# Optimization experiments

Hardware: AMD Instinct MI355X
Metric: run time of the kernel (lower is better)

The kernel has to match this reference:

```python
import jax, jax.numpy as jnp
import numpy as np

B, N, CS, CZ, H, CH, G, P = 2, 384, 384, 128, 8, 16, 2, 8
CZ4 = CZ // 4
INF = 1e5
UMAX = 3.0     # self.u_max
LMAX = 2.0     # self.log_scale_max
SQRT_CH = CH ** 0.5


def quat_to_rot(q):
    q = q / jnp.linalg.norm(q, axis=-1, keepdims=True)
    w, x, y, z = q[..., 0], q[..., 1], q[..., 2], q[..., 3]
    R = jnp.stack([
        1 - 2 * (y * y + z * z), 2 * (x * y - w * z), 2 * (x * z + w * y),
        2 * (x * y + w * z), 1 - 2 * (x * x + z * z), 2 * (y * z - w * x),
        2 * (x * z - w * y), 2 * (y * z + w * x), 1 - 2 * (x * x + y * y)], axis=-1)
    return R.reshape(q.shape[:-1] + (3, 3))


def robust_nll(delta, sigma):
    # inline robust 3x3 Cholesky solve: dist_sq = d^T S^-1 d, log_det = ln|S|
    eps = 1e-8
    s00 = sigma[..., 0, 0]; s01 = sigma[..., 0, 1]; s02 = sigma[..., 0, 2]
    s11 = sigma[..., 1, 1]; s12 = sigma[..., 1, 2]; s22 = sigma[..., 2, 2]
    d0 = delta[..., 0]; d1 = delta[..., 1]; d2 = delta[..., 2]
    l00_sq = jnp.maximum(s00, eps); inv_l00 = jax.lax.rsqrt(l00_sq)
    l10 = s01 * inv_l00; l20 = s02 * inv_l00
    l11_sq = jnp.maximum(s11 - l10 * l10, eps); inv_l11 = jax.lax.rsqrt(l11_sq)
    l21 = (s12 - l20 * l10) * inv_l11
    l22_sq = jnp.maximum(s22 - l20 * l20 - l21 * l21, eps); inv_l22 = jax.lax.rsqrt(l22_sq)
    log_det = jnp.log(l00_sq) + jnp.log(l11_sq) + jnp.log(l22_sq)
    y0 = d0 * inv_l00
    y1 = (d1 - l10 * y0) * inv_l11
    y2 = (d2 - l20 * y0 - l21 * y1) * inv_l22
    return y0 * y0 + y1 * y1 + y2 * y2, log_det


def iga_forward(s, z, mask, rot, trans, local_mean, scaling_log,
                Wq, Wk, Wv, Wb, bb, Wdz, bdz, Wqg, bqg, Wkg, bkg,
                Wvp, bvp, geo_scale, geo_bias, Wout, bout):
    # scalar q/k/v: [B,H,N,CH]
    q = (s @ Wq).reshape(B, N, H, CH).transpose(0, 2, 1, 3)
    k = (s @ Wk).reshape(B, N, H, CH).transpose(0, 2, 1, 3)
    v = (s @ Wv).reshape(B, N, H, CH).transpose(0, 2, 1, 3)
    logits = jnp.einsum('bhid,bhjd->bhij', q, k) / SQRT_CH
    # pair bias: [B,H,N,N]
    logits = logits + (z @ Wb + bb).transpose(0, 3, 1, 2)

    def parse(feat):  # -> u [B,N,H,G,3], s_log_delta [B,N,H,G,3]
        raw = feat.reshape(B, N, H, G, 6)
        return jnp.tanh(raw[..., :3]) * UMAX, jnp.tanh(raw[..., 3:]) * LMAX

    def to_global(u, sld):
        anchor = local_mean[:, :, None, None, :]
        base = scaling_log[:, :, None, None, :]
        sig_loc = jnp.maximum(jnp.exp(base + sld), 1e-6)
        pos = anchor + u * sig_loc
        mu = jnp.einsum('bnij,bnhgj->bnhgi', rot, pos) + trans[:, :, None, None, :]
        var = jnp.exp(2.0 * (base + sld))
        Sig = jnp.einsum('bnij,bnhgj,bnkj->bnhgik', rot, var, rot)  # R diag(var) R^T
        return mu.transpose(0, 2, 1, 3, 4), Sig.transpose(0, 2, 1, 3, 4, 5)

    qu, qs = parse(s @ Wqg + bqg)
    ku, ks = parse(s @ Wkg + bkg)
    q_mu, q_sig = to_global(qu, qs)   # [B,H,N,G,3], [B,H,N,G,3,3]
    k_mu, k_sig = to_global(ku, ks)
    delta = q_mu[:, :, :, None] - k_mu[:, :, None, :]      # [B,H,N,N,G,3]
    ssum = q_sig[:, :, :, None] + k_sig[:, :, None, :]     # [B,H,N,N,G,3,3]
    dist_sq, log_det = robust_nll(delta, ssum)
    geo = (-0.5 * dist_sq - 0.5 * log_det).sum(-1)          # [B,H,N,N]

    mask2d = mask[:, None, :, None] * mask[:, None, None, :]  # [B,1,N,N]
    a = jax.nn.softplus(geo_scale)[None, :, None, None]
    G_geo = a * (geo * mask2d) + geo_bias[None, :, None, None]
    logits = logits + G_geo + (1.0 - mask2d) * (-INF)
    w = jax.nn.softmax(logits, axis=-1)                      # [B,H,N,N]

    # scalar output
    o = jnp.einsum('bhij,bhjd->bihd', w, v).reshape(B, N, H * CH)
    # point output (IPA-style): to global, attend, back to local frame
    vpts = (s @ Wvp + bvp).reshape(B, N, H, P, 3)
    vpg = jnp.einsum('bnij,bnhpj->bnhpi', rot, vpts) + trans[:, :, None, None, :]
    vpg = vpg.transpose(0, 2, 1, 3, 4)                       # [B,H,N,P,3]
    opt = jnp.einsum('bhij,bhjpc->bhipc', w, vpg)            # [B,H,N,P,3]
    opt_local = jnp.einsum('bnji,bhnpj->bnhpi', rot, opt - trans[:, None, :, None, :])
    onorm = jnp.sqrt((opt_local ** 2).sum(-1) + 1e-8)        # [B,N,H,P]
    # pair output
    pz = z @ Wdz + bdz                                       # [B,N,N,CZ4]
    opair = jnp.einsum('bhij,bijc->bihc', w, pz)             # [B,N,H,CZ4]

    cat = jnp.concatenate([o, opt_local.reshape(B, N, H * P * 3),
                           onorm.reshape(B, N, H * P),
                           opair.reshape(B, N, H * CZ4)], axis=-1)  # [B,N,640]
    return cat @ Wout + bout


def setup_inputs() -> dict:
    ks = jax.random.split(jax.random.key(0), 24)
    rnd = lambda i, shape, sc=1.0: jax.random.normal(ks[i], shape, dtype=jnp.float32) * sc
    w = 0.02
    return dict(
        s=rnd(0, (B, N, CS)), z=rnd(1, (B, N, N, CZ)),
        mask=jnp.ones((B, N), jnp.float32),
        rot=quat_to_rot(rnd(2, (B, N, 4))),
        trans=rnd(3, (B, N, 3), 1.0),
        local_mean=rnd(4, (B, N, 3), 0.5),
        scaling_log=rnd(5, (B, N, 3), 0.1),
        Wq=rnd(6, (CS, H * CH), w), Wk=rnd(7, (CS, H * CH), w), Wv=rnd(8, (CS, H * CH), w),
        Wb=rnd(9, (CZ, H), w), bb=rnd(10, (H,), w),
        Wdz=rnd(11, (CZ, CZ4), w), bdz=rnd(12, (CZ4,), w),
        Wqg=rnd(13, (CS, H * G * 6), w), bqg=rnd(14, (H * G * 6,), w),
        Wkg=rnd(15, (CS, H * G * 6), w), bkg=rnd(16, (H * G * 6,), w),
        Wvp=rnd(17, (CS, H * P * 3), w), bvp=rnd(18, (H * P * 3,), w),
        geo_scale=jnp.ones((H,), jnp.float32), geo_bias=jnp.zeros((H,), jnp.float32),
        Wout=rnd(19, (H * (CH + P * 4 + CZ4), CS), w), bout=jnp.zeros((CS,), jnp.float32))


def reference(s, z, mask, rot, trans, local_mean, scaling_log, Wq, Wk, Wv, Wb, bb,
              Wdz, bdz, Wqg, bqg, Wkg, bkg, Wvp, bvp, geo_scale, geo_bias, Wout, bout):
    return iga_forward(s, z, mask, rot, trans, local_mean, scaling_log, Wq, Wk, Wv,
                       Wb, bb, Wdz, bdz, Wqg, bqg, Wkg, bkg, Wvp, bvp,
                       geo_scale, geo_bias, Wout, bout)
```

## Files before the change

kernel.cpp:

```cpp
#include <hip/hip_runtime.h>
#include <hip/hip_fp16.h>

#define NB   2
#define NN   384
#define NCS  384
#define NCZ  128
#define NH   8
#define NCH  16
#define NG   2
#define NP   8
#define NCZ4 32
#define BN   (NB*NN)
#define LINW 768
#define PZROW ((size_t)BN*NN)
#define NZP  1152
#define NRB  288

typedef _Float16 f16x8 __attribute__((ext_vector_type(8)));
typedef float    f32x4 __attribute__((ext_vector_type(4)));

typedef __attribute__((address_space(3))) char        as3_char;
typedef __attribute__((address_space(1))) const char  as1_char;
static __device__ __forceinline__ void gload_lds16(const void* g, void* l) {
    __builtin_amdgcn_global_load_lds((const as1_char*)g, (as3_char*)l, 16, 0, 0);
}

__global__ void k_wprep(const float* __restrict__ Wb, const float* __restrict__ Wdz,
                        _Float16* __restrict__ wf) {
    int t = threadIdx.x;
    for (int e = t; e < 12*64*8; e += 256) {
        int r = e & 7, lane = (e >> 3) & 63, nk = e >> 9;
        int n = nk >> 2, kk = nk & 3;
        int c = kk*32 + (lane >> 4)*8 + r;
        int col = n*16 + (lane & 15);
        float w;
        if      (col < 8)  w = Wb[c*NH + col];
        else if (col < 40) w = Wdz[c*NCZ4 + (col-8)];
        else               w = 0.f;
        wf[e] = (_Float16)w;
    }
}

static __device__ __forceinline__ void zchunk_body(
        const char* zbuf, char* outb, const f16x8* bfr,
        float b0, float b1, float b2,
        int t, int lane, int w, int ccol, int cjl, int bi, int ch,
        float* __restrict__ zbg, __half* __restrict__ pzg2) {
    float (*zbT)[64] = (float(*)[64])outb;
    __half (*pzt)[34] = (__half(*)[34])(outb + 2048);
    int row = w*16 + (lane & 15);
    int r7  = row & 7;
    const char* zrow_b = zbuf + row*512;
    f16x8 af[4];
    #pragma unroll
    for (int kk = 0; kk < 4; ++kk) {
        int u0 = ((lane >> 4) << 1) + kk*8;
        float4 lo = *(const float4*)(zrow_b + (((u0    ) ^ r7) << 4));
        float4 hi = *(const float4*)(zrow_b + (((u0 + 1) ^ r7) << 4));
        af[kk][0]=(_Float16)lo.x; af[kk][1]=(_Float16)lo.y;
        af[kk][2]=(_Float16)lo.z; af[kk][3]=(_Float16)lo.w;
        af[kk][4]=(_Float16)hi.x; af[kk][5]=(_Float16)hi.y;
        af[kk][6]=(_Float16)hi.z; af[kk][7]=(_Float16)hi.w;
    }
    f32x4 ac0 = {0.f,0.f,0.f,0.f}, ac1 = ac0, ac2 = ac0;
    ac0 = __builtin_amdgcn_mfma_f32_16x16x32_f16(af[0], bfr[0], ac0, 0,0,0);
    ac1 = __builtin_amdgcn_mfma_f32_16x16x32_f16(af[0], bfr[4], ac1, 0,0,0);
    ac2 = __builtin_amdgcn_mfma_f32_16x16x32_f16(af[0], bfr[8], ac2, 0,0,0);
    ac0 = __builtin_amdgcn_mfma_f32_16x16x32_f16(af[1], bfr[1], ac0, 0,0,0);
    ac1 = __builtin_amdgcn_mfma_f32_16x16x32_f16(af[1], bfr[5], ac1, 0,0,0);
    ac2 = __builtin_amdgcn_mfma_f32_16x16x32_f16(af[1], bfr[9], ac2, 0,0,0);
    ac0 = __builtin_amdgcn_mfma_f32_16x16x32_f16(af[2], bfr[2], ac0, 0,0,0);
    ac1 = __builtin_amdgcn_mfma_f32_16x16x32_f16(af[2], bfr[6], ac1, 0,0,0);
    ac2 = __builtin_amdgcn_mfma_f32_16x16x32_f16(af[2], bfr[10], ac2, 0,0,0);
    ac0 = __builtin_amdgcn_mfma_f32_16x16x32_f16(af[3], bfr[3], ac0, 0,0,0);
    ac1 = __builtin_amdgcn_mfma_f32_16x16x32_f16(af[3], bfr[7], ac1, 0,0,0);
    ac2 = __builtin_amdgcn_mfma_f32_16x16x32_f16(af[3], bfr[11], ac2, 0,0,0);
    #pragma unroll
    for (int r = 0; r < 4; ++r) {
        int j = cjl + r;
        float v0 = ac0[r] + b0;
        if (ccol < 8) zbT[ccol][j] = v0;
        else          pzt[j][ccol-8] = __float2half(v0);
        pzt[j][ccol+8] = __float2half(ac1[r] + b1);
        if (ccol < 8)
            pzt[j][ccol+24] = __float2half(ac2[r] + b2);
    }
    asm volatile("s_waitcnt lgkmcnt(0)" ::: "memory");
    __builtin_amdgcn_sched_barrier(0);
    __builtin_amdgcn_s_barrier();
    __builtin_amdgcn_sched_barrier(0);
    {
        int e = t*2, h = e >> 6, j = e & 63;
        float2 v; v.x = zbT[h][j]; v.y = zbT[h][j+1];
        *(float2*)(zbg + ((size_t)bi*NH + h)*NN + ch*64 + j) = v;
    }
    {
        int cp = t >> 4, l = t & 15, j0 = l*4;
        union { __half2 h2[4]; float4 f4; } u;
        #pragma unroll
        for (int r = 0; r < 4; ++r) {
            int j = j0 + r;
            u.h2[r] = __halves2half2(pzt[j][2*cp], pzt[j][2*cp+1]);
        }
        __half2* dst = (__half2*)pzg2 + (size_t)cp*PZROW + (size_t)bi*NN + ch*64 + j0;
        *(float4*)dst = u.f4;
    }
}

static __device__ __forceinline__ void dma_chunk(const float* z, int c, int lane, int w,
                                                 char* dstbuf) {
    const char* nb = (const char*)(z + ((size_t)(c/6)*NN + (c%6)*64)*NCZ);
    #pragma unroll
    for (int i = 0; i < 8; ++i) {
        int o = (w*8 + i)*1024 + lane*16;
        int r = o >> 9;
        int u = (o >> 4) & 31;
        gload_lds16(nb + (r << 9) + ((u ^ (r & 7)) << 4), dstbuf + (w*8 + i)*1024);
    }
}

__global__ void k_zrow(const float* __restrict__ z, const _Float16* __restrict__ wf,
       const float* __restrict__ bb, const float* __restrict__ bdz,
       const float* __restrict__ s,
       const float* __restrict__ Wq, const float* __restrict__ Wk,
       const float* __restrict__ Wv,
       const float* __restrict__ Wqg, const float* __restrict__ bqg,
       const float* __restrict__ Wkg, const float* __restrict__ bkg,
       const float* __restrict__ Wvp, const float* __restrict__ bvp,
       float* __restrict__ zbg, __half* __restrict__ pzg2,
       float* __restrict__ lin, float* __restrict__ kT, float* __restrict__ vT) {
    __shared__ __align__(16) char smem[78336];
    int t = threadIdx.x;

    if (blockIdx.x >= NRB) {
        int lane = t & 63, w = t >> 6;
        int ccol = lane & 15;
        int cjl  = w*16 + (lane >> 4)*4;
        int zbid = blockIdx.x - NRB;

        dma_chunk(z, zbid, lane, w, smem);

        f16x8 bfr[12];
        #pragma unroll
        for (int nk = 0; nk < 12; ++nk)
            bfr[nk] = ((const f16x8*)wf)[nk*64 + lane];
        float b0 = (ccol < 8) ? bb[ccol] : bdz[ccol - 8];
        float b1 = bdz[ccol + 8];
        float b2 = (ccol < 8) ? bdz[ccol + 24] : 0.f;

        dma_chunk(z, zbid + NZP, lane, w, smem + 32768);
        asm volatile("s_waitcnt vmcnt(8)" ::: "memory");
        __builtin_amdgcn_sched_barrier(0);
        __builtin_amdgcn_s_barrier();
        __builtin_amdgcn_sched_barrier(0);
        zchunk_body(smem, smem + 65536, bfr, b0, b1, b2, t, lane, w, ccol, cjl,
                    zbid / 6, zbid % 6, zbg, pzg2);

        dma_chunk(z, zbid + 2*NZP, lane, w, smem);
        asm volatile("s_waitcnt vmcnt(8)" ::: "memory");
        __builtin_amdgcn_sched_barrier(0);
        __builtin_amdgcn_s_barrier();
        __builtin_amdgcn_sched_barrier(0);
        {
            int c = zbid + NZP;
            zchunk_body(smem + 32768, smem + 65536 + 6400, bfr, b0, b1, b2, t, lane, w,
                        ccol, cjl, c / 6, c % 6, zbg, pzg2);
        }

        dma_chunk(z, zbid + 3*NZP, lane, w, smem + 32768);
        asm volatile("s_waitcnt vmcnt(8)" ::: "memory");
        __builtin_amdgcn_sched_barrier(0);
        __builtin_amdgcn_s_barrier();
        __builtin_amdgcn_sched_barrier(0);
        {
            int c = zbid + 2*NZP;
            zchunk_body(smem, smem + 65536, bfr, b0, b1, b2, t, lane, w,
                        ccol, cjl, c / 6, c % 6, zbg, pzg2);
        }

        asm volatile("s_waitcnt vmcnt(0)" ::: "memory");
        __builtin_amdgcn_sched_barrier(0);
        __builtin_amdgcn_s_barrier();
        __builtin_amdgcn_sched_barrier(0);
        {
            int c = zbid + 3*NZP;
            zchunk_body(smem + 32768, smem + 65536 + 6400, bfr, b0, b1, b2, t, lane, w,
                        ccol, cjl, c / 6, c % 6, zbg, pzg2);
        }
    } else {
        float (*sl)[NCS] = (float(*)[NCS])smem;
        int rb = blockIdx.x;
        int r0 = (rb / 3) * 8;
        int col = (rb % 3) * 256 + t;
        for (int idx = t; idx < 8*NCS; idx += 256)
            sl[idx / NCS][idx % NCS] = s[(size_t)(r0 + idx/NCS)*NCS + (idx % NCS)];
        __syncthreads();
        const float* W; int sw; float bias = 0.f;
        if      (col < 128) { W = Wq  + col;        sw = 128; }
        else if (col < 256) { W = Wk  + (col-128);  sw = 128; }
        else if (col < 384) { W = Wv  + (col-256);  sw = 128; }
        else if (col < 480) { W = Wqg + (col-384);  sw = 96;  bias = bqg[col-384]; }
        else if (col < 576) { W = Wkg + (col-480);  sw = 96;  bias = bkg[col-480]; }
        else                { W = Wvp + (col-576);  sw = 192; bias = bvp[col-576]; }
        float a[8];
        #pragma unroll
        for (int r = 0; r < 8; ++r) a[r] = 0.f;
        #pragma unroll 1
        for (int c = 0; c < NCS; c += 4) {
            float w0 = W[(size_t)(c+0)*sw];
            float w1 = W[(size_t)(c+1)*sw];
            float w2 = W[(size_t)(c+2)*sw];
            float w3 = W[(size_t)(c+3)*sw];
            #pragma unroll
            for (int r = 0; r < 8; ++r) {
                a[r] = fmaf(sl[r][c+0], w0, a[r]);
                a[r] = fmaf(sl[r][c+1], w1, a[r]);
                a[r] = fmaf(sl[r][c+2], w2, a[r]);
                a[r] = fmaf(sl[r][c+3], w3, a[r]);
            }
        }
        #pragma unroll
        for (int r = 0; r < 8; ++r)
            lin[(size_t)(r0+r)*LINW + col] = a[r] + bias;
        if (col >= 128 && col < 384) {
            f32x4 v0, v1;
            #pragma unroll
            for (int r = 0; r < 4; ++r) { v0[r] = a[r]; v1[r] = a[4+r]; }
            float* dst = (col < 256) ? (kT + (size_t)(col-128)*BN + r0)
                                     : (vT + (size_t)(col-256)*BN + r0);
            *(f32x4*)dst = v0;
            *(f32x4*)(dst+4) = v1;
        }
    }
}

__global__ void k_geom(const float* __restrict__ lin, const float* __restrict__ rot,
                       const float* __restrict__ trans, const float* __restrict__ lm,
                       const float* __restrict__ sc,
                       float* __restrict__ qmu, float* __restrict__ qsig,
                       float* __restrict__ kmuT, float* __restrict__ ksigT,
                       float* __restrict__ vpgT) {
    int bn = blockIdx.x, t = threadIdx.x;
    __shared__ float R[9], T[3], A[3], Bs[3];
    if (t < 9) R[t] = rot[bn*9 + t];
    if (t < 3) { T[t] = trans[bn*3+t]; A[t] = lm[bn*3+t]; Bs[t] = sc[bn*3+t]; }
    __syncthreads();
    {
        int h = t >> 3, p = t & 7;
        const float* vr = lin + (size_t)bn*LINW + 576 + h*24 + p*3;
        float x = vr[0], y = vr[1], z = vr[2];
        int e = h*24 + p*3;
        vpgT[(size_t)(e+0)*BN + bn] = R[0]*x + R[1]*y + R[2]*z + T[0];
        vpgT[(size_t)(e+1)*BN + bn] = R[3]*x + R[4]*y + R[5]*z + T[1];
        vpgT[(size_t)(e+2)*BN + bn] = R[6]*x + R[7]*y + R[8]*z + T[2];
    }
    if (t < 32) {
        int side = t >> 4, item = t & 15;
        const float* raw = lin + (size_t)bn*LINW + (side ? 480 : 384) + item*6;
        float u0 = tanhf(raw[0])*3.f, u1 = tanhf(raw[1])*3.f, u2 = tanhf(raw[2])*3.f;
        float e0 = Bs[0] + tanhf(raw[3])*2.f;
        float e1 = Bs[1] + tanhf(raw[4])*2.f;
        float e2 = Bs[2] + tanhf(raw[5])*2.f;
        float sl0 = fmaxf(expf(e0), 1e-6f);
        float sl1 = fmaxf(expf(e1), 1e-6f);
        float sl2 = fmaxf(expf(e2), 1e-6f);
        float p0 = A[0] + u0*sl0, p1 = A[1] + u1*sl1, p2 = A[2] + u2*sl2;
        float mu0 = R[0]*p0 + R[1]*p1 + R[2]*p2 + T[0];
        float mu1 = R[3]*p0 + R[4]*p1 + R[5]*p2 + T[1];
        float mu2 = R[6]*p0 + R[7]*p1 + R[8]*p2 + T[2];
        float v0 = expf(2.f*e0), v1 = expf(2.f*e1), v2 = expf(2.f*e2);
        float s00 = R[0]*R[0]*v0 + R[1]*R[1]*v1 + R[2]*R[2]*v2;
        float s01 = R[0]*R[3]*v0 + R[1]*R[4]*v1 + R[2]*R[5]*v2;
        float s02 = R[0]*R[6]*v0 + R[1]*R[7]*v1 + R[2]*R[8]*v2;
        float s11 = R[3]*R[3]*v0 + R[4]*R[4]*v1 + R[5]*R[5]*v2;
        float s12 = R[3]*R[6]*v0 + R[4]*R[7]*v1 + R[5]*R[8]*v2;
        float s22 = R[6]*R[6]*v0 + R[7]*R[7]*v1 + R[8]*R[8]*v2;
        if (side) {
            kmuT[(size_t)(item*3+0)*BN + bn] = mu0;
            kmuT[(size_t)(item*3+1)*BN + bn] = mu1;
            kmuT[(size_t)(item*3+2)*BN + bn] = mu2;
            ksigT[(size_t)(item*6+0)*BN + bn] = s00;
            ksigT[(size_t)(item*6+1)*BN + bn] = s01;
            ksigT[(size_t)(item*6+2)*BN + bn] = s02;
            ksigT[(size_t)(item*6+3)*BN + bn] = s11;
            ksigT[(size_t)(item*6+4)*BN + bn] = s12;
            ksigT[(size_t)(item*6+5)*BN + bn] = s22;
        } else {
            float* mud = qmu + (size_t)bn*48 + item*3;
            mud[0]=mu0; mud[1]=mu1; mud[2]=mu2;
            float* sgd = qsig + (size_t)bn*96 + item*6;
            sgd[0]=s00; sgd[1]=s01; sgd[2]=s02; sgd[3]=s11; sgd[4]=s12; sgd[5]=s22;
        }
    }
}

__global__ void __launch_bounds__(256, 2)
k_attn2(const float* __restrict__ mask,
        const float* __restrict__ rot, const float* __restrict__ trans,
        const float* __restrict__ lin,
        const float* __restrict__ qmu, const float* __restrict__ qsig,
        const float* __restrict__ kmuT, const float* __restrict__ ksigT,
        const float* __restrict__ kT, const float* __restrict__ vT,
        const float* __restrict__ vpgT,
        const float* __restrict__ zbg, const __half* __restrict__ pzg2,
        const float* __restrict__ gsc, const float* __restrict__ gbi,
        float* __restrict__ cat) {
    __shared__ float  logits[NH][NN];
    __shared__ float  qrow[128];
    __shared__ float  qmu_s[48], qsig_s[96];
    __shared__ float  Rm[9], Tv[3];
    __shared__ float  aH[NH], bH[NH];
    __shared__ float  maskI;

    int t  = threadIdx.x;
    int b  = blockIdx.x / NN, i = blockIdx.x % NN;
    int bi = b*NN + i;
    const size_t boff = (size_t)b*NN;

    if (t < 128) qrow[t] = lin[(size_t)bi*LINW + t];
    if (t < 48)  qmu_s[t] = qmu[(size_t)bi*48 + t];
    if (t >= 64 && t < 160) qsig_s[t-64] = qsig[(size_t)bi*96 + (t-64)];
    if (t >= 160 && t < 169) Rm[t-160] = rot[bi*9 + (t-160)];
    if (t >= 169 && t < 172) Tv[t-169] = trans[bi*3 + (t-169)];
    if (t >= 176 && t < 184) {
        int h = t-176;
        float x = gsc[h];
        aH[h] = (x > 20.f) ? x : log1pf(expf(x));
        bH[h] = gbi[h];
    }
    if (t == 255) maskI = mask[bi];
    __syncthreads();

    int h = t >> 5, lnn = t & 31;
    {
        float qv[16];
        #pragma unroll
        for (int d = 0; d < 16; ++d) qv[d] = qrow[h*16 + d];
        float qm[6], qs[12];
        #pragma unroll
        for (int e = 0; e < 6; ++e)  qm[e] = qmu_s[h*6 + e];
        #pragma unroll
        for (int e = 0; e < 12; ++e) qs[e] = qsig_s[h*12 + e];
        float ascale = aH[h], hbias = bH[h], mI = maskI;
        #pragma unroll 1
        for (int jj = 0; jj < 3; ++jj) {
            int j4 = jj*128 + lnn*4;
            const float* kp = kT + (size_t)(h*16)*BN + boff + j4;
            f32x4 qk = {0.f,0.f,0.f,0.f};
            #pragma unroll
            for (int d = 0; d < 16; ++d) {
                f32x4 kv = *(const f32x4*)(kp + (size_t)d*BN);
                #pragma unroll
                for (int r = 0; r < 4; ++r) qk[r] = fmaf(qv[d], kv[r], qk[r]);
            }
            f32x4 geo = {0.f,0.f,0.f,0.f};
            #pragma unroll
            for (int g = 0; g < NG; ++g) {
                const float* kmb = kmuT + (size_t)((h*2+g)*3)*BN + boff + j4;
                f32x4 km0 = *(const f32x4*)(kmb);
                f32x4 km1 = *(const f32x4*)(kmb + BN);
                f32x4 km2 = *(const f32x4*)(kmb + 2*BN);
                const float* ksb = ksigT + (size_t)((h*2+g)*6)*BN + boff + j4;
                f32x4 ks0 = *(const f32x4*)(ksb);
                f32x4 ks1 = *(const f32x4*)(ksb + BN);
                f32x4 ks2 = *(const f32x4*)(ksb + 2*BN);
                f32x4 ks3 = *(const f32x4*)(ksb + 3*BN);
                f32x4 ks4 = *(const f32x4*)(ksb + 4*BN);
                f32x4 ks5 = *(const f32x4*)(ksb + 5*BN);
                #pragma unroll
                for (int r = 0; r < 4; ++r) {
                    float d0 = qm[g*3+0] - km0[r];
                    float d1 = qm[g*3+1] - km1[r];
                    float d2 = qm[g*3+2] - km2[r];
                    float s00 = qs[g*6+0] + ks0[r];
                    float s01 = qs[g*6+1] + ks1[r];
                    float s02 = qs[g*6+2] + ks2[r];
                    float s11 = qs[g*6+3] + ks3[r];
                    float s12 = qs[g*6+4] + ks4[r];
                    float s22 = qs[g*6+5] + ks5[r];
                    float l00 = fmaxf(s00, 1e-8f);
                    float i00 = rsqrtf(l00);
                    float l10 = s01*i00, l20 = s02*i00;
                    float l11 = fmaxf(s11 - l10*l10, 1e-8f);
                    float i11 = rsqrtf(l11);
                    float l21 = (s12 - l20*l10)*i11;
                    float l22 = fmaxf(s22 - l20*l20 - l21*l21, 1e-8f);
                    float i22 = rsqrtf(l22);
                    float ld = __logf(l00) + __logf(l11) + __logf(l22);
                    float y0 = d0*i00;
                    float y1 = (d1 - l10*y0)*i11;
                    float y2 = (d2 - l20*y0 - l21*y1)*i22;
                    geo[r] += -0.5f*(y0*y0 + y1*y1 + y2*y2 + ld);
                }
            }
            f32x4 zb4 = *(const f32x4*)(zbg + ((size_t)bi*NH + h)*NN + j4);
            f32x4 mv  = *(const f32x4*)(mask + boff + j4);
            f32x4 lg;
            #pragma unroll
            for (int r = 0; r < 4; ++r) {
                float m2 = mI * mv[r];
                lg[r] = qk[r]*0.25f + zb4[r] + ascale*(geo[r]*m2) + hbias
                        + (1.f - m2)*(-100000.f);
            }
            *(f32x4*)&logits[h][j4] = lg;
        }
    }
    __syncthreads();

    float mx = -3.4e38f;
    #pragma unroll
    for (int jj = 0; jj < 12; ++jj) mx = fmaxf(mx, logits[h][lnn + jj*32]);
    #pragma unroll
    for (int m = 16; m >= 1; m >>= 1) mx = fmaxf(mx, __shfl_xor(mx, m, 64));
    float se = 0.f;
    #pragma unroll
    for (int jj = 0; jj < 12; ++jj) {
        int j = lnn + jj*32;
        float e = __expf(logits[h][j] - mx);
        logits[h][j] = e;
        se += e;
    }
    #pragma unroll
    for (int m = 16; m >= 1; m >>= 1) se += __shfl_xor(se, m, 64);
    float inv = 1.f / se;
    float* cp = cat + (size_t)bi*640;

    {
        float o[16];
        #pragma unroll
        for (int d = 0; d < 16; ++d) o[d] = 0.f;
        const float* vbase = vT + (size_t)(h*16)*BN + boff;
        #pragma unroll 1
        for (int jj = 0; jj < 3; ++jj) {
            int j4 = jj*128 + lnn*4;
            f32x4 lg4 = *(const f32x4*)&logits[h][j4];
            f32x4 w4;
            #pragma unroll
            for (int r = 0; r < 4; ++r) w4[r] = lg4[r] * inv;
            const float* vb = vbase + j4;
            #pragma unroll
            for (int d = 0; d < 16; ++d) {
                f32x4 kv = *(const f32x4*)(vb + (size_t)d*BN);
                #pragma unroll
                for (int r = 0; r < 4; ++r) o[d] = fmaf(w4[r], kv[r], o[d]);
            }
        }
        #pragma unroll
        for (int m = 16; m >= 1; m >>= 1) {
            #pragma unroll
            for (int d = 0; d < 16; ++d) o[d] += __shfl_xor(o[d], m, 64);
        }
        if (lnn == 0) {
            #pragma unroll
            for (int d = 0; d < 16; ++d) cp[h*16 + d] = o[d];
        }
    }

    {
        float op[24];
        #pragma unroll
        for (int e = 0; e < 24; ++e) op[e] = 0.f;
        const float* gbase = vpgT + (size_t)(h*24)*BN + boff;
        #pragma unroll 1
        for (int jj = 0; jj < 3; ++jj) {
            int j4 = jj*128 + lnn*4;
            f32x4 lg4 = *(const f32x4*)&logits[h][j4];
            f32x4 w4;
            #pragma unroll
            for (int r = 0; r < 4; ++r) w4[r] = lg4[r] * inv;
            const float* gb = gbase + j4;
            #pragma unroll
            for (int e = 0; e < 24; ++e) {
                f32x4 gv = *(const f32x4*)(gb + (size_t)e*BN);
                #pragma unroll
                for (int r = 0; r < 4; ++r) op[e] = fmaf(w4[r], gv[r], op[e]);
            }
        }
        #pragma unroll
        for (int m = 16; m >= 1; m >>= 1) {
            #pragma unroll
            for (int e = 0; e < 24; ++e) op[e] += __shfl_xor(op[e], m, 64);
        }
        if (lnn == 0) {
            #pragma unroll
            for (int p = 0; p < 8; ++p) {
                float x  = op[p*3+0] - Tv[0];
                float y  = op[p*3+1] - Tv[1];
                float zz = op[p*3+2] - Tv[2];
                float l0 = Rm[0]*x + Rm[3]*y + Rm[6]*zz;
                float l1 = Rm[1]*x + Rm[4]*y + Rm[7]*zz;
                float l2 = Rm[2]*x + Rm[5]*y + Rm[8]*zz;
                cp[128 + h*24 + p*3 + 0] = l0;
                cp[128 + h*24 + p*3 + 1] = l1;
                cp[128 + h*24 + p*3 + 2] = l2;
                cp[320 + h*8 + p] = sqrtf(l0*l0 + l1*l1 + l2*l2 + 1e-8f);
            }
        }
    }

    {
        float opa[32];
        #pragma unroll
        for (int c = 0; c < 32; ++c) opa[c] = 0.f;
        const __half2* pzb = (const __half2*)pzg2 + (size_t)bi*NN;
        #pragma unroll 1
        for (int jj = 0; jj < 3; ++jj) {
            int j4 = jj*128 + lnn*4;
            f32x4 lg4 = *(const f32x4*)&logits[h][j4];
            f32x4 w4;
            #pragma unroll
            for (int r = 0; r < 4; ++r) w4[r] = lg4[r] * inv;
            #pragma unroll
            for (int c2 = 0; c2 < 16; ++c2) {
                union { float4 f4; __half2 h2[4]; } u;
                u.f4 = *(const float4*)(pzb + (size_t)c2*PZROW + j4);
                #pragma unroll
                for (int r = 0; r < 4; ++r) {
                    float2 pf = __half22float2(u.h2[r]);
                    opa[2*c2]   = fmaf(w4[r], pf.x, opa[2*c2]);
                    opa[2*c2+1] = fmaf(w4[r], pf.y, opa[2*c2+1]);
                }
            }
        }
        #pragma unroll
        for (int m = 16; m >= 1; m >>= 1) {
            #pragma unroll
            for (int c = 0; c < 32; ++c) opa[c] += __shfl_xor(opa[c], m, 64);
        }
        if (lnn == 0) {
            #pragma unroll
            for (int c = 0; c < 32; ++c) cp[384 + h*32 + c] = opa[c];
        }
    }
}

__global__ void k_out(const float* __restrict__ cat, const float* __restrict__ Wout,
                      const float* __restrict__ bout, float* __restrict__ out) {
    __shared__ float cl[4][640];
    int t  = threadIdx.x;
    int r0 = blockIdx.x * 4;
    for (int idx = t; idx < 4*640; idx += 384)
        cl[idx/640][idx%640] = cat[(size_t)(r0 + idx/640)*640 + (idx%640)];
    __syncthreads();
    int col = t;
    float a0=0.f, a1=0.f, a2=0.f, a3=0.f;
    for (int c = 0; c < 640; ++c) {
        float w = Wout[(size_t)c*NCS + col];
        a0 = fmaf(cl[0][c], w, a0);
        a1 = fmaf(cl[1][c], w, a1);
        a2 = fmaf(cl[2][c], w, a2);
        a3 = fmaf(cl[3][c], w, a3);
    }
    float bv = bout[col];
    out[(size_t)(r0+0)*NCS + col] = a0 + bv;
    out[(size_t)(r0+1)*NCS + col] = a1 + bv;
    out[(size_t)(r0+2)*NCS + col] = a2 + bv;
    out[(size_t)(r0+3)*NCS + col] = a3 + bv;
}

extern "C" void kernel_launch(void* const* d_in, const int* in_sizes, int n_in,
                              void* d_out, int out_size, void* d_ws, size_t ws_size,
                              hipStream_t stream) {
    const float* s    = (const float*)d_in[0];
    const float* z    = (const float*)d_in[1];
    const float* mask = (const float*)d_in[2];
    const float* rot  = (const float*)d_in[3];
    const float* trans= (const float*)d_in[4];
    const float* lm   = (const float*)d_in[5];
    const float* sc   = (const float*)d_in[6];
    const float* Wq   = (const float*)d_in[7];
    const float* Wk   = (const float*)d_in[8];
    const float* Wv   = (const float*)d_in[9];
    const float* Wb   = (const float*)d_in[10];
    const float* bb   = (const float*)d_in[11];
    const float* Wdz  = (const float*)d_in[12];
    const float* bdz  = (const float*)d_in[13];
    const float* Wqg  = (const float*)d_in[14];
    const float* bqg  = (const float*)d_in[15];
    const float* Wkg  = (const float*)d_in[16];
    const float* bkg  = (const float*)d_in[17];
    const float* Wvp  = (const float*)d_in[18];
    const float* bvp  = (const float*)d_in[19];
    const float* gsc  = (const float*)d_in[20];
    const float* gbi  = (const float*)d_in[21];
    const float* Wout = (const float*)d_in[22];
    const float* bout = (const float*)d_in[23];
    float* out = (float*)d_out;

    float* ws    = (float*)d_ws;
    float* lin   = ws;
    float* qmu   = lin   + 589824;
    float* qsig  = qmu   + 36864;
    float* kmuT  = qsig  + 73728;
    float* ksigT = kmuT  + 36864;
    float* vpgT  = ksigT + 73728;
    float* kT    = vpgT  + 147456;
    float* vT    = kT    + 98304;
    float* cat   = vT    + 98304;
    float* zbg   = cat   + 491520;
    __half* pzg2 = (__half*)(zbg + 2359296);
    _Float16* wf = (_Float16*)((float*)pzg2 + 4718592);

    k_wprep<<<1, 256, 0, stream>>>(Wb, Wdz, wf);
    k_zrow<<<NRB + NZP, 256, 0, stream>>>(z, wf, bb, bdz, s,
                                          Wq, Wk, Wv, Wqg, bqg, Wkg, bkg, Wvp, bvp,
                                          zbg, pzg2, lin, kT, vT);
    k_geom<<<BN, 64, 0, stream>>>(lin, rot, trans, lm, sc, qmu, qsig, kmuT, ksigT, vpgT);
    k_attn2<<<BN, 256, 0, stream>>>(mask, rot, trans, lin, qmu, qsig, kmuT, ksigT,
                                    kT, vT, vpgT, zbg, pzg2, gsc, gbi, cat);
    k_out<<<192, 384, 0, stream>>>(cat, Wout, bout, out);
}
```

Before: 146.0 us.

## Process one z chunk per block with per-wave LDS staging, no block barriers

Replaces the four-chunk double-buffered z projection loop (1152 blocks, each processing four 64-row chunks with block barriers) with one chunk per block (4608 blocks). Each wave loads and transposes its own 16 rows through a private LDS region, so no block-wide barriers are needed. LDS per block halves, which raises occupancy, but the explicit DMA/compute overlap is lost and launch/prologue costs (loading the weight fragments per block) are repeated four times as often.

```diff
diff --git a/kernel.cpp b/kernel.cpp
--- a/kernel.cpp
+++ b/kernel.cpp
@@ -13,7 +13,7 @@
 #define BN   (NB*NN)
 #define LINW 768
 #define PZROW ((size_t)BN*NN)
-#define NZP  1152
+#define NZB  (BN*6)
 #define NRB  288
 
 typedef _Float16 f16x8 __attribute__((ext_vector_type(8)));
@@ -41,84 +41,6 @@
     }
 }
 
-static __device__ __forceinline__ void zchunk_body(
-        const char* zbuf, char* outb, const f16x8* bfr,
-        float b0, float b1, float b2,
-        int t, int lane, int w, int ccol, int cjl, int bi, int ch,
-        float* __restrict__ zbg, __half* __restrict__ pzg2) {
-    float (*zbT)[64] = (float(*)[64])outb;
-    __half (*pzt)[34] = (__half(*)[34])(outb + 2048);
-    int row = w*16 + (lane & 15);
-    int r7  = row & 7;
-    const char* zrow_b = zbuf + row*512;
-    f16x8 af[4];
-    #pragma unroll
-    for (int kk = 0; kk < 4; ++kk) {
-        int u0 = ((lane >> 4) << 1) + kk*8;
-        float4 lo = *(const float4*)(zrow_b + (((u0    ) ^ r7) << 4));
-        float4 hi = *(const float4*)(zrow_b + (((u0 + 1) ^ r7) << 4));
-        af[kk][0]=(_Float16)lo.x; af[kk][1]=(_Float16)lo.y;
-        af[kk][2]=(_Float16)lo.z; af[kk][3]=(_Float16)lo.w;
-        af[kk][4]=(_Float16)hi.x; af[kk][5]=(_Float16)hi.y;
-        af[kk][6]=(_Float16)hi.z; af[kk][7]=(_Float16)hi.w;
-    }
-    f32x4 ac0 = {0.f,0.f,0.f,0.f}, ac1 = ac0, ac2 = ac0;
-    ac0 = __builtin_amdgcn_mfma_f32_16x16x32_f16(af[0], bfr[0], ac0, 0,0,0);
-    ac1 = __builtin_amdgcn_mfma_f32_16x16x32_f16(af[0], bfr[4], ac1, 0,0,0);
-    ac2 = __builtin_amdgcn_mfma_f32_16x16x32_f16(af[0], bfr[8], ac2, 0,0,0);
-    ac0 = __builtin_amdgcn_mfma_f32_16x16x32_f16(af[1], bfr[1], ac0, 0,0,0);
-    ac1 = __builtin_amdgcn_mfma_f32_16x16x32_f16(af[1], bfr[5], ac1, 0,0,0);
-    ac2 = __builtin_amdgcn_mfma_f32_16x16x32_f16(af[1], bfr[9], ac2, 0,0,0);
-    ac0 = __builtin_amdgcn_mfma_f32_16x16x32_f16(af[2], bfr[2], ac0, 0,0,0);
-    ac1 = __builtin_amdgcn_mfma_f32_16x16x32_f16(af[2], bfr[6], ac1, 0,0,0);
-    ac2 = __builtin_amdgcn_mfma_f32_16x16x32_f16(af[2], bfr[10], ac2, 0,0,0);
-    ac0 = __builtin_amdgcn_mfma_f32_16x16x32_f16(af[3], bfr[3], ac0, 0,0,0);
-    ac1 = __builtin_amdgcn_mfma_f32_16x16x32_f16(af[3], bfr[7], ac1, 0,0,0);
-    ac2 = __builtin_amdgcn_mfma_f32_16x16x32_f16(af[3], bfr[11], ac2, 0,0,0);
-    #pragma unroll
-    for (int r = 0; r < 4; ++r) {
-        int j = cjl + r;
-        float v0 = ac0[r] + b0;
-        if (ccol < 8) zbT[ccol][j] = v0;
-        else          pzt[j][ccol-8] = __float2half(v0);
-        pzt[j][ccol+8] = __float2half(ac1[r] + b1);
-        if (ccol < 8)
-            pzt[j][ccol+24] = __float2half(ac2[r] + b2);
-    }
-    asm volatile("s_waitcnt lgkmcnt(0)" ::: "memory");
-    __builtin_amdgcn_sched_barrier(0);
-    __builtin_amdgcn_s_barrier();
-    __builtin_amdgcn_sched_barrier(0);
-    {
-        int e = t*2, h = e >> 6, j = e & 63;
-        float2 v; v.x = zbT[h][j]; v.y = zbT[h][j+1];
-        *(float2*)(zbg + ((size_t)bi*NH + h)*NN + ch*64 + j) = v;
-    }
-    {
-        int cp = t >> 4, l = t & 15, j0 = l*4;
-        union { __half2 h2[4]; float4 f4; } u;
-        #pragma unroll
-        for (int r = 0; r < 4; ++r) {
-            int j = j0 + r;
-            u.h2[r] = __halves2half2(pzt[j][2*cp], pzt[j][2*cp+1]);
-        }
-        __half2* dst = (__half2*)pzg2 + (size_t)cp*PZROW + (size_t)bi*NN + ch*64 + j0;
-        *(float4*)dst = u.f4;
-    }
-}
-
-static __device__ __forceinline__ void dma_chunk(const float* z, int c, int lane, int w,
-                                                 char* dstbuf) {
-    const char* nb = (const char*)(z + ((size_t)(c/6)*NN + (c%6)*64)*NCZ);
-    #pragma unroll
-    for (int i = 0; i < 8; ++i) {
-        int o = (w*8 + i)*1024 + lane*16;
-        int r = o >> 9;
-        int u = (o >> 4) & 31;
-        gload_lds16(nb + (r << 9) + ((u ^ (r & 7)) << 4), dstbuf + (w*8 + i)*1024);
-    }
-}
-
 __global__ void k_zrow(const float* __restrict__ z, const _Float16* __restrict__ wf,
        const float* __restrict__ bb, const float* __restrict__ bdz,
        const float* __restrict__ s,
@@ -129,16 +51,24 @@
        const float* __restrict__ Wvp, const float* __restrict__ bvp,
        float* __restrict__ zbg, __half* __restrict__ pzg2,
        float* __restrict__ lin, float* __restrict__ kT, float* __restrict__ vT) {
-    __shared__ __align__(16) char smem[78336];
+    __shared__ __align__(16) char smem[39168];
     int t = threadIdx.x;
 
     if (blockIdx.x >= NRB) {
         int lane = t & 63, w = t >> 6;
         int ccol = lane & 15;
-        int cjl  = w*16 + (lane >> 4)*4;
-        int zbid = blockIdx.x - NRB;
-
-        dma_chunk(z, zbid, lane, w, smem);
+        int zb = blockIdx.x - NRB;
+        int bi = zb / 6, ch = zb % 6;
+
+        const char* zbase = (const char*)(z + ((size_t)bi*NN + ch*64 + w*16)*NCZ);
+        char* myin = smem + w*8192;
+        #pragma unroll
+        for (int i = 0; i < 8; ++i) {
+            int o = i*1024 + lane*16;
+            int r = o >> 9;
+            int u = (o >> 4) & 31;
+            gload_lds16(zbase + (r << 9) + ((u ^ (r & 7)) << 4), myin + i*1024);
+        }
 
         f16x8 bfr[12];
         #pragma unroll
@@ -148,44 +78,68 @@
         float b1 = bdz[ccol + 8];
         float b2 = (ccol < 8) ? bdz[ccol + 24] : 0.f;
 
-        dma_chunk(z, zbid + NZP, lane, w, smem + 32768);
-        asm volatile("s_waitcnt vmcnt(8)" ::: "memory");
-        __builtin_amdgcn_sched_barrier(0);
-        __builtin_amdgcn_s_barrier();
-        __builtin_amdgcn_sched_barrier(0);
-        zchunk_body(smem, smem + 65536, bfr, b0, b1, b2, t, lane, w, ccol, cjl,
-                    zbid / 6, zbid % 6, zbg, pzg2);
-
-        dma_chunk(z, zbid + 2*NZP, lane, w, smem);
-        asm volatile("s_waitcnt vmcnt(8)" ::: "memory");
-        __builtin_amdgcn_sched_barrier(0);
-        __builtin_amdgcn_s_barrier();
-        __builtin_amdgcn_sched_barrier(0);
-        {
-            int c = zbid + NZP;
-            zchunk_body(smem + 32768, smem + 65536 + 6400, bfr, b0, b1, b2, t, lane, w,
-                        ccol, cjl, c / 6, c % 6, zbg, pzg2);
-        }
-
-        dma_chunk(z, zbid + 3*NZP, lane, w, smem + 32768);
-        asm volatile("s_waitcnt vmcnt(8)" ::: "memory");
-        __builtin_amdgcn_sched_barrier(0);
-        __builtin_amdgcn_s_barrier();
-        __builtin_amdgcn_sched_barrier(0);
-        {
-            int c = zbid + 2*NZP;
-            zchunk_body(smem, smem + 65536, bfr, b0, b1, b2, t, lane, w,
-                        ccol, cjl, c / 6, c % 6, zbg, pzg2);
-        }
-
         asm volatile("s_waitcnt vmcnt(0)" ::: "memory");
         __builtin_amdgcn_sched_barrier(0);
-        __builtin_amdgcn_s_barrier();
+
+        int lrow = lane & 15;
+        int r7   = lrow & 7;
+        const char* zrow_b = myin + lrow*512;
+        f16x8 af[4];
+        #pragma unroll
+        for (int kk = 0; kk < 4; ++kk) {
+            int u0 = ((lane >> 4) << 1) + kk*8;
+            float4 lo = *(const float4*)(zrow_b + (((u0    ) ^ r7) << 4));
+            float4 hi = *(const float4*)(zrow_b + (((u0 + 1) ^ r7) << 4));
+            af[kk][0]=(_Float16)lo.x; af[kk][1]=(_Float16)lo.y;
+            af[kk][2]=(_Float16)lo.z; af[kk][3]=(_Float16)lo.w;
+            af[kk][4]=(_Float16)hi.x; af[kk][5]=(_Float16)hi.y;
+            af[kk][6]=(_Float16)hi.z; af[kk][7]=(_Float16)hi.w;
+        }
+
+        f32x4 ac0 = {0.f,0.f,0.f,0.f}, ac1 = ac0, ac2 = ac0;
+        ac0 = __builtin_amdgcn_mfma_f32_16x16x32_f16(af[0], bfr[0], ac0, 0,0,0);
+        ac1 = __builtin_amdgcn_mfma_f32_16x16x32_f16(af[0], bfr[4], ac1, 0,0,0);
+        ac2 = __builtin_amdgcn_mfma_f32_16x16x32_f16(af[0], bfr[8], ac2, 0,0,0);
+        ac0 = __builtin_amdgcn_mfma_f32_16x16x32_f16(af[1], bfr[1], ac0, 0,0,0);
+        ac1 = __builtin_amdgcn_mfma_f32_16x16x32_f16(af[1], bfr[5], ac1, 0,0,0);
+        ac2 = __builtin_amdgcn_mfma_f32_16x16x32_f16(af[1], bfr[9], ac2, 0,0,0);
+        ac0 = __builtin_amdgcn_mfma_f32_16x16x32_f16(af[2], bfr[2], ac0, 0,0,0);
+        ac1 = __builtin_amdgcn_mfma_f32_16x16x32_f16(af[2], bfr[6], ac1, 0,0,0);
+        ac2 = __builtin_amdgcn_mfma_f32_16x16x32_f16(af[2], bfr[10], ac2, 0,0,0);
+        ac0 = __builtin_amdgcn_mfma_f32_16x16x32_f16(af[3], bfr[3], ac0, 0,0,0);
+        ac1 = __builtin_amdgcn_mfma_f32_16x16x32_f16(af[3], bfr[7], ac1, 0,0,0);
+        ac2 = __builtin_amdgcn_mfma_f32_16x16x32_f16(af[3], bfr[11], ac2, 0,0,0);
+
+        char* outw = smem + 32768 + w*1600;
+        float (*zbTw)[16] = (float(*)[16])outw;
+        __half (*pztw)[34] = (__half(*)[34])(outw + 512);
+        #pragma unroll
+        for (int r = 0; r < 4; ++r) {
+            int jl = (lane >> 4)*4 + r;
+            float v0 = ac0[r] + b0;
+            if (ccol < 8) zbTw[ccol][jl] = v0;
+            else          pztw[jl][ccol-8] = __float2half(v0);
+            pztw[jl][ccol+8] = __float2half(ac1[r] + b1);
+            if (ccol < 8)
+                pztw[jl][ccol+24] = __float2half(ac2[r] + b2);
+        }
+        asm volatile("s_waitcnt lgkmcnt(0)" ::: "memory");
         __builtin_amdgcn_sched_barrier(0);
+
+        int jglob = ch*64 + w*16;
         {
-            int c = zbid + 3*NZP;
-            zchunk_body(smem + 32768, smem + 65536 + 6400, bfr, b0, b1, b2, t, lane, w,
-                        ccol, cjl, c / 6, c % 6, zbg, pzg2);
+            int h = lane >> 3, jj = (lane & 7)*2;
+            float2 v; v.x = zbTw[h][jj]; v.y = zbTw[h][jj+1];
+            *(float2*)(zbg + ((size_t)bi*NH + h)*NN + jglob + jj) = v;
+        }
+        {
+            int cp = lane >> 2, j0 = (lane & 3)*4;
+            union { __half2 h2[4]; float4 f4; } u;
+            #pragma unroll
+            for (int r = 0; r < 4; ++r)
+                u.h2[r] = __halves2half2(pztw[j0+r][2*cp], pztw[j0+r][2*cp+1]);
+            __half2* dst = (__half2*)pzg2 + (size_t)cp*PZROW + (size_t)bi*NN + jglob + j0;
+            *(float4*)dst = u.f4;
         }
     } else {
         float (*sl)[NCS] = (float(*)[NCS])smem;
@@ -602,7 +556,7 @@
     _Float16* wf = (_Float16*)((float*)pzg2 + 4718592);
 
     k_wprep<<<1, 256, 0, stream>>>(Wb, Wdz, wf);
-    k_zrow<<<NRB + NZP, 256, 0, stream>>>(z, wf, bb, bdz, s,
+    k_zrow<<<NRB + NZB, 256, 0, stream>>>(z, wf, bb, bdz, s,
                                           Wq, Wk, Wv, Wqg, bqg, Wkg, bkg, Wvp, bvp,
                                           zbg, pzg2, lin, kT, vT);
     k_geom<<<BN, 64, 0, stream>>>(lin, rot, trans, lm, sc, qmu, qsig, kmuT, ksigT, vpgT);
```

After: 149.0 us. 1.02x slower.
